# Performance work log

Measured on AMD Instinct MI355X. Metric: run time of the kernel, lower is better.

## Reference

```python
import jax, jax.numpy as jnp
import numpy as np

VOCAB = 50257
EMB = 100
BOT = 5  # bottleneck dim of the tiny autoencoder MLP


def setup_inputs() -> dict:
    key = jax.random.key(0)
    ks = jax.random.split(key, 7)
    B, S = 128, 2048
    x = jax.random.randint(ks[0], (B, S), 0, VOCAB, dtype=jnp.int64)
    word_embed = jax.random.normal(ks[1], (VOCAB, EMB), dtype=jnp.float32)
    # idf values are positive; use uniform(0,1] scaled up a bit to mimic log-idf
    idf = jax.random.uniform(ks[2], (VOCAB,), dtype=jnp.float32, minval=0.01, maxval=10.0)
    fc1_w = jax.random.normal(ks[3], (BOT, EMB), dtype=jnp.float32) * (1.0 / np.sqrt(EMB))
    fc1_b = jax.random.normal(ks[4], (BOT,), dtype=jnp.float32) * 0.01
    fc2_w = jax.random.normal(ks[5], (EMB, BOT), dtype=jnp.float32) * (1.0 / np.sqrt(BOT))
    fc2_b = jax.random.normal(ks[6], (EMB,), dtype=jnp.float32) * 0.01
    return {"x": x, "word_embed": word_embed, "idf": idf,
            "fc1_w": fc1_w, "fc1_b": fc1_b, "fc2_w": fc2_w, "fc2_b": fc2_b}


def reference(x, word_embed, idf, fc1_w, fc1_b, fc2_w, fc2_b):
    B, S = x.shape
    V = idf.shape[0]
    # tf(): per-row token histogram. Equivalent math to the torch dense
    # one-hot scatter + sum over seq, done as a scatter-add (no (B,S,V) tensor).
    rows = jnp.broadcast_to(jnp.arange(B)[:, None], (B, S))
    tf = jnp.zeros((B, V), dtype=jnp.float32).at[rows, x].add(1.0)
    # tf-idf weights, row-normalized
    tfidf = tf * idf[None, :]
    tfidf = tfidf / jnp.sum(tfidf, axis=1, keepdims=True)
    # per-token weight: gather each row's tfidf at its token ids  -> [B, S]
    w = jnp.take_along_axis(tfidf, x, axis=1)
    # embedding lookup and tfidf-weighted sum over seq  -> [B, EMB]
    emb = word_embed[x]  # [B, S, EMB]
    doc = jnp.einsum('bse,bs->be', emb, w)
    # tiny 100 -> 5 -> 100 MLP (no nonlinearity in the original)
    h = doc @ fc1_w.T + fc1_b
    out = h @ fc2_w.T + fc2_b
    return out
```

## Files before the change

### kernel.cpp

```cpp
#include <hip/hip_runtime.h>

#define SEQ   2048
#define HALF  1024
#define EMB   100
#define BOT   5
#define HSIZE 4096
#define FT    1024
#define NW    16
#define GW    12
#define GTOK  76
#define HTOK  28

__global__ __launch_bounds__(FT) void kA_fused(
    const int* __restrict__ x, const float* __restrict__ idf,
    const float* __restrict__ we, float* __restrict__ partial,
    float* __restrict__ zhalf)
{
    __shared__ int   hkey[HSIZE];
    __shared__ int   hcnt[HSIZE];
    __shared__ int   skey[SEQ];
    __shared__ float sdup[HALF];
    __shared__ float part[NW][EMB];
    __shared__ float zred[NW];

    const int bx   = blockIdx.x;
    const int b    = bx >> 1;
    const int half = bx & 1;
    const int tid  = threadIdx.x;
    const int lane = tid & 63, wid = tid >> 6;
    const int vl   = (lane < EMB / 2) ? lane : 0;

    for (int i = tid; i < HSIZE; i += FT) { hkey[i] = -1; hcnt[i] = 0; }
    for (int i = tid; i < SEQ; i += FT) skey[i] = x[(size_t)b * SEQ + i];
    __syncthreads();

    if (wid >= GW) {
        const int ht = tid - GW * 64;
        for (int i = ht; i < SEQ; i += (NW - GW) * 64) {
            int key = skey[i];
            unsigned slot = ((unsigned)key * 2654435761u) >> 20;
            for (;;) {
                int prev = atomicCAS(&hkey[slot], -1, key);
                if (prev == -1 || prev == key) { atomicAdd(&hcnt[slot], 1); break; }
                slot = (slot + 1) & (HSIZE - 1);
            }
        }
    }

    const int hb    = half * HALF;
    const int start = (wid < GW) ? wid * GTOK : GW * GTOK + (wid - GW) * HTOK;
    const int end   = start + ((wid < GW) ? GTOK : HTOK);

    float accx, accy;
    float z = 0.0f;
    {
        float2 a0={0,0},a1={0,0},a2={0,0},a3={0,0},a4={0,0},a5={0,0},a6={0,0},a7={0,0};
        int i = start;
        for (; i + 8 <= end; i += 8) {
            int   k0=skey[hb+i+0], k1=skey[hb+i+1], k2=skey[hb+i+2], k3=skey[hb+i+3];
            int   k4=skey[hb+i+4], k5=skey[hb+i+5], k6=skey[hb+i+6], k7=skey[hb+i+7];
            float w0=idf[k0], w1=idf[k1], w2=idf[k2], w3=idf[k3];
            float w4=idf[k4], w5=idf[k5], w6=idf[k6], w7=idf[k7];
            float2 v0=((const float2*)(we+(size_t)k0*EMB))[vl];
            float2 v1=((const float2*)(we+(size_t)k1*EMB))[vl];
            float2 v2=((const float2*)(we+(size_t)k2*EMB))[vl];
            float2 v3=((const float2*)(we+(size_t)k3*EMB))[vl];
            float2 v4=((const float2*)(we+(size_t)k4*EMB))[vl];
            float2 v5=((const float2*)(we+(size_t)k5*EMB))[vl];
            float2 v6=((const float2*)(we+(size_t)k6*EMB))[vl];
            float2 v7=((const float2*)(we+(size_t)k7*EMB))[vl];
            a0.x+=w0*v0.x; a0.y+=w0*v0.y;  a1.x+=w1*v1.x; a1.y+=w1*v1.y;
            a2.x+=w2*v2.x; a2.y+=w2*v2.y;  a3.x+=w3*v3.x; a3.y+=w3*v3.y;
            a4.x+=w4*v4.x; a4.y+=w4*v4.y;  a5.x+=w5*v5.x; a5.y+=w5*v5.y;
            a6.x+=w6*v6.x; a6.y+=w6*v6.y;  a7.x+=w7*v7.x; a7.y+=w7*v7.y;
            z += ((w0+w1)+(w2+w3)) + ((w4+w5)+(w6+w7));
        }
        for (; i < end; ++i) {
            int k = skey[hb+i];
            float w = idf[k];
            float2 v = ((const float2*)(we+(size_t)k*EMB))[vl];
            a0.x += w*v.x; a0.y += w*v.y; z += w;
        }
        accx = ((a0.x+a1.x)+(a2.x+a3.x)) + ((a4.x+a5.x)+(a6.x+a7.x));
        accy = ((a0.y+a1.y)+(a2.y+a3.y)) + ((a4.y+a5.y)+(a6.y+a7.y));
    }
    if (lane == 0) zred[wid] = z;
    __syncthreads();

    {
        int k = skey[hb + tid];
        unsigned slot = ((unsigned)k * 2654435761u) >> 20;
        while (hkey[slot] != k) slot = (slot + 1) & (HSIZE - 1);
        int c = hcnt[slot];
        sdup[tid] = (c > 1) ? (float)(c - 1) * idf[k] : 0.0f;
    }
    __syncthreads();

    {
        float wl = sdup[wid * 64 + lane];
        int   kl = skey[hb + wid * 64 + lane];
        unsigned long long m = __ballot(wl != 0.0f);
        while (m) {
            int src = __ffsll((long long)m) - 1;  m &= m - 1;
            float w = __shfl(wl, src);
            int   k = __shfl(kl, src);
            float2 v = ((const float2*)(we + (size_t)k * EMB))[vl];
            accx += w * v.x; accy += w * v.y;
        }
    }
    if (lane < EMB / 2) { part[wid][2*lane] = accx; part[wid][2*lane+1] = accy; }
    __syncthreads();

    if (tid < EMB) {
        float a = 0.0f;
        #pragma unroll
        for (int w = 0; w < NW; ++w) a += part[w][tid];
        partial[(size_t)bx * EMB + tid] = a;
    }
    if (tid == 0) {
        float t = 0.0f;
        #pragma unroll
        for (int w = 0; w < NW; ++w) t += zred[w];
        zhalf[bx] = t;
    }
}

__global__ __launch_bounds__(128) void kB_mlp(
    const float* __restrict__ partial, const float* __restrict__ zhalf,
    const float* __restrict__ fc1w, const float* __restrict__ fc1b,
    const float* __restrict__ fc2w, const float* __restrict__ fc2b,
    float* __restrict__ out)
{
    __shared__ float doc[EMB];
    __shared__ float hsh[BOT];

    const int b = blockIdx.x, tid = threadIdx.x;
    const float iz = 1.0f / (zhalf[2*b] + zhalf[2*b+1]);

    if (tid < EMB) {
        const float* p = partial + (size_t)b * 2 * EMB + tid;
        doc[tid] = (p[0] + p[EMB]) * iz;
    }
    __syncthreads();

    if (tid < BOT) {
        float h = fc1b[tid];
        const float* wr = fc1w + tid * EMB;
        for (int e = 0; e < EMB; ++e) h += doc[e] * wr[e];
        hsh[tid] = h;
    }
    __syncthreads();

    if (tid < EMB) {
        float o = fc2b[tid];
        const float* wr = fc2w + tid * BOT;
        #pragma unroll
        for (int j = 0; j < BOT; ++j) o += hsh[j] * wr[j];
        out[(size_t)b * EMB + tid] = o;
    }
}

extern "C" void kernel_launch(void* const* d_in, const int* in_sizes, int n_in,
                              void* d_out, int out_size, void* d_ws, size_t ws_size,
                              hipStream_t stream) {
    const int*   x    = (const int*)d_in[0];
    const float* we   = (const float*)d_in[1];
    const float* idf  = (const float*)d_in[2];
    const float* fc1w = (const float*)d_in[3];
    const float* fc1b = (const float*)d_in[4];
    const float* fc2w = (const float*)d_in[5];
    const float* fc2b = (const float*)d_in[6];
    float*       out  = (float*)d_out;

    const int B = in_sizes[0] / SEQ;

    char*  ws      = (char*)d_ws;
    float* zhalf   = (float*)ws;
    float* partial = (float*)(ws + 4096);

    kA_fused<<<B * 2, FT,  0, stream>>>(x, idf, we, partial, zhalf);
    kB_mlp  <<<B,     128, 0, stream>>>(partial, zhalf, fc1w, fc1b, fc2w, fc2b, out);
}
```

Baseline: 98.29 us.

## Restructure histogram and gather: all warps hash, float4 gathers, cached idf in LDS

Every thread now inserts two tokens into the shared hash table and keeps their slots, so the separate lookup probe pass is gone. The idf values are loaded once into shared memory and the normaliser is reduced with wave shuffles. The embedding gather switches from float2 to float4 loads, with two tokens per wave (25 lanes each), spread evenly over all 16 warps. Each block now computes the full-row normaliser redundantly, so the second kernel reads it directly. Duplicate correction leaves lanes 25-63 idle, and shared memory use grows.

```diff
diff --git a/kernel.cpp b/kernel.cpp
--- a/kernel.cpp
+++ b/kernel.cpp
@@ -7,126 +7,136 @@
 #define HSIZE 4096
 #define FT    1024
 #define NW    16
-#define GW    12
-#define GTOK  76
-#define HTOK  28
 
 __global__ __launch_bounds__(FT) void kA_fused(
     const int* __restrict__ x, const float* __restrict__ idf,
     const float* __restrict__ we, float* __restrict__ partial,
-    float* __restrict__ zhalf)
+    float* __restrict__ zfull)
 {
     __shared__ int   hkey[HSIZE];
     __shared__ int   hcnt[HSIZE];
     __shared__ int   skey[SEQ];
+    __shared__ float sidf[SEQ];
     __shared__ float sdup[HALF];
-    __shared__ float part[NW][EMB];
+    __shared__ float part[NW][2][EMB];
     __shared__ float zred[NW];
 
-    const int bx   = blockIdx.x;
-    const int b    = bx >> 1;
-    const int half = bx & 1;
-    const int tid  = threadIdx.x;
-    const int lane = tid & 63, wid = tid >> 6;
-    const int vl   = (lane < EMB / 2) ? lane : 0;
+    const int bx = blockIdx.x, b = bx >> 1, half = bx & 1;
+    const int tid = threadIdx.x, lane = tid & 63, wid = tid >> 6;
 
     for (int i = tid; i < HSIZE; i += FT) { hkey[i] = -1; hcnt[i] = 0; }
-    for (int i = tid; i < SEQ; i += FT) skey[i] = x[(size_t)b * SEQ + i];
+    skey[tid]        = x[(size_t)b * SEQ + tid];
+    skey[tid + HALF] = x[(size_t)b * SEQ + tid + HALF];
     __syncthreads();
 
-    if (wid >= GW) {
-        const int ht = tid - GW * 64;
-        for (int i = ht; i < SEQ; i += (NW - GW) * 64) {
-            int key = skey[i];
-            unsigned slot = ((unsigned)key * 2654435761u) >> 20;
-            for (;;) {
-                int prev = atomicCAS(&hkey[slot], -1, key);
-                if (prev == -1 || prev == key) { atomicAdd(&hcnt[slot], 1); break; }
-                slot = (slot + 1) & (HSIZE - 1);
+    const int   k0 = skey[tid], k1 = skey[tid + HALF];
+    const float w0 = idf[k0],   w1 = idf[k1];
+
+    unsigned slot0 = ((unsigned)k0 * 2654435761u) >> 20;
+    for (;;) {
+        int prev = atomicCAS(&hkey[slot0], -1, k0);
+        if (prev == -1 || prev == k0) { atomicAdd(&hcnt[slot0], 1); break; }
+        slot0 = (slot0 + 1) & (HSIZE - 1);
+    }
+    unsigned slot1 = ((unsigned)k1 * 2654435761u) >> 20;
+    for (;;) {
+        int prev = atomicCAS(&hkey[slot1], -1, k1);
+        if (prev == -1 || prev == k1) { atomicAdd(&hcnt[slot1], 1); break; }
+        slot1 = (slot1 + 1) & (HSIZE - 1);
+    }
+
+    sidf[tid] = w0;  sidf[tid + HALF] = w1;
+
+    float z = w0 + w1;
+    for (int off = 32; off > 0; off >>= 1) z += __shfl_down(z, off);
+    if (lane == 0) zred[wid] = z;
+    __syncthreads();
+
+    {
+        const int   ms = half ? (int)slot1 : (int)slot0;
+        const float mw = half ? w1 : w0;
+        const int   c  = hcnt[ms];
+        sdup[tid] = (c > 1) ? (float)(c - 1) * mw : 0.0f;
+    }
+    if (tid == 0) {
+        float t = 0.0f;
+        #pragma unroll
+        for (int i = 0; i < NW; ++i) t += zred[i];
+        zfull[b] = t;
+    }
+    __syncthreads();
+
+    const int  hb  = half * HALF;
+    const bool act = (lane < 50);
+    const int  sub = (lane < 25) ? 0 : 1;
+    const int  q   = (lane < 25) ? lane : lane - 25;
+
+    float4 a0={0,0,0,0}, a1={0,0,0,0}, a2={0,0,0,0}, a3={0,0,0,0};
+    float4 a4={0,0,0,0}, a5={0,0,0,0}, a6={0,0,0,0}, a7={0,0,0,0};
+
+    if (act) {
+        const int t0 = hb + wid * 64 + sub;
+        #pragma unroll
+        for (int it = 0; it < 4; ++it) {
+            const int base = t0 + it * 16;
+            int   kk0 = skey[base+ 0], kk1 = skey[base+ 2], kk2 = skey[base+ 4], kk3 = skey[base+ 6];
+            int   kk4 = skey[base+ 8], kk5 = skey[base+10], kk6 = skey[base+12], kk7 = skey[base+14];
+            float ww0 = sidf[base+ 0], ww1 = sidf[base+ 2], ww2 = sidf[base+ 4], ww3 = sidf[base+ 6];
+            float ww4 = sidf[base+ 8], ww5 = sidf[base+10], ww6 = sidf[base+12], ww7 = sidf[base+14];
+            float4 v0 = ((const float4*)(we + (size_t)kk0 * EMB))[q];
+            float4 v1 = ((const float4*)(we + (size_t)kk1 * EMB))[q];
+            float4 v2 = ((const float4*)(we + (size_t)kk2 * EMB))[q];
+            float4 v3 = ((const float4*)(we + (size_t)kk3 * EMB))[q];
+            float4 v4 = ((const float4*)(we + (size_t)kk4 * EMB))[q];
+            float4 v5 = ((const float4*)(we + (size_t)kk5 * EMB))[q];
+            float4 v6 = ((const float4*)(we + (size_t)kk6 * EMB))[q];
+            float4 v7 = ((const float4*)(we + (size_t)kk7 * EMB))[q];
+            a0.x+=ww0*v0.x; a0.y+=ww0*v0.y; a0.z+=ww0*v0.z; a0.w+=ww0*v0.w;
+            a1.x+=ww1*v1.x; a1.y+=ww1*v1.y; a1.z+=ww1*v1.z; a1.w+=ww1*v1.w;
+            a2.x+=ww2*v2.x; a2.y+=ww2*v2.y; a2.z+=ww2*v2.z; a2.w+=ww2*v2.w;
+            a3.x+=ww3*v3.x; a3.y+=ww3*v3.y; a3.z+=ww3*v3.z; a3.w+=ww3*v3.w;
+            a4.x+=ww4*v4.x; a4.y+=ww4*v4.y; a4.z+=ww4*v4.z; a4.w+=ww4*v4.w;
+            a5.x+=ww5*v5.x; a5.y+=ww5*v5.y; a5.z+=ww5*v5.z; a5.w+=ww5*v5.w;
+            a6.x+=ww6*v6.x; a6.y+=ww6*v6.y; a6.z+=ww6*v6.z; a6.w+=ww6*v6.w;
+            a7.x+=ww7*v7.x; a7.y+=ww7*v7.y; a7.z+=ww7*v7.z; a7.w+=ww7*v7.w;
+        }
+    }
+
+    {
+        float sd = sdup[wid * 64 + lane];
+        int   kl = skey[hb + wid * 64 + lane];
+        unsigned long long m = __ballot(sd != 0.0f);
+        while (m) {
+            int src = __ffsll((long long)m) - 1;  m &= m - 1;
+            float wv = __shfl(sd, src);
+            int   kv = __shfl(kl, src);
+            if (lane < 25) {
+                float4 v = ((const float4*)(we + (size_t)kv * EMB))[q];
+                a0.x += wv*v.x; a0.y += wv*v.y; a0.z += wv*v.z; a0.w += wv*v.w;
             }
         }
     }
 
-    const int hb    = half * HALF;
-    const int start = (wid < GW) ? wid * GTOK : GW * GTOK + (wid - GW) * HTOK;
-    const int end   = start + ((wid < GW) ? GTOK : HTOK);
-
-    float accx, accy;
-    float z = 0.0f;
-    {
-        float2 a0={0,0},a1={0,0},a2={0,0},a3={0,0},a4={0,0},a5={0,0},a6={0,0},a7={0,0};
-        int i = start;
-        for (; i + 8 <= end; i += 8) {
-            int   k0=skey[hb+i+0], k1=skey[hb+i+1], k2=skey[hb+i+2], k3=skey[hb+i+3];
-            int   k4=skey[hb+i+4], k5=skey[hb+i+5], k6=skey[hb+i+6], k7=skey[hb+i+7];
-            float w0=idf[k0], w1=idf[k1], w2=idf[k2], w3=idf[k3];
-            float w4=idf[k4], w5=idf[k5], w6=idf[k6], w7=idf[k7];
-            float2 v0=((const float2*)(we+(size_t)k0*EMB))[vl];
-            float2 v1=((const float2*)(we+(size_t)k1*EMB))[vl];
-            float2 v2=((const float2*)(we+(size_t)k2*EMB))[vl];
-            float2 v3=((const float2*)(we+(size_t)k3*EMB))[vl];
-            float2 v4=((const float2*)(we+(size_t)k4*EMB))[vl];
-            float2 v5=((const float2*)(we+(size_t)k5*EMB))[vl];
-            float2 v6=((const float2*)(we+(size_t)k6*EMB))[vl];
-            float2 v7=((const float2*)(we+(size_t)k7*EMB))[vl];
-            a0.x+=w0*v0.x; a0.y+=w0*v0.y;  a1.x+=w1*v1.x; a1.y+=w1*v1.y;
-            a2.x+=w2*v2.x; a2.y+=w2*v2.y;  a3.x+=w3*v3.x; a3.y+=w3*v3.y;
-            a4.x+=w4*v4.x; a4.y+=w4*v4.y;  a5.x+=w5*v5.x; a5.y+=w5*v5.y;
-            a6.x+=w6*v6.x; a6.y+=w6*v6.y;  a7.x+=w7*v7.x; a7.y+=w7*v7.y;
-            z += ((w0+w1)+(w2+w3)) + ((w4+w5)+(w6+w7));
-        }
-        for (; i < end; ++i) {
-            int k = skey[hb+i];
-            float w = idf[k];
-            float2 v = ((const float2*)(we+(size_t)k*EMB))[vl];
-            a0.x += w*v.x; a0.y += w*v.y; z += w;
-        }
-        accx = ((a0.x+a1.x)+(a2.x+a3.x)) + ((a4.x+a5.x)+(a6.x+a7.x));
-        accy = ((a0.y+a1.y)+(a2.y+a3.y)) + ((a4.y+a5.y)+(a6.y+a7.y));
+    if (act) {
+        float4 s;
+        s.x = ((a0.x+a1.x)+(a2.x+a3.x)) + ((a4.x+a5.x)+(a6.x+a7.x));
+        s.y = ((a0.y+a1.y)+(a2.y+a3.y)) + ((a4.y+a5.y)+(a6.y+a7.y));
+        s.z = ((a0.z+a1.z)+(a2.z+a3.z)) + ((a4.z+a5.z)+(a6.z+a7.z));
+        s.w = ((a0.w+a1.w)+(a2.w+a3.w)) + ((a4.w+a5.w)+(a6.w+a7.w));
+        ((float4*)part[wid][sub])[q] = s;
     }
-    if (lane == 0) zred[wid] = z;
-    __syncthreads();
-
-    {
-        int k = skey[hb + tid];
-        unsigned slot = ((unsigned)k * 2654435761u) >> 20;
-        while (hkey[slot] != k) slot = (slot + 1) & (HSIZE - 1);
-        int c = hcnt[slot];
-        sdup[tid] = (c > 1) ? (float)(c - 1) * idf[k] : 0.0f;
-    }
-    __syncthreads();
-
-    {
-        float wl = sdup[wid * 64 + lane];
-        int   kl = skey[hb + wid * 64 + lane];
-        unsigned long long m = __ballot(wl != 0.0f);
-        while (m) {
-            int src = __ffsll((long long)m) - 1;  m &= m - 1;
-            float w = __shfl(wl, src);
-            int   k = __shfl(kl, src);
-            float2 v = ((const float2*)(we + (size_t)k * EMB))[vl];
-            accx += w * v.x; accy += w * v.y;
-        }
-    }
-    if (lane < EMB / 2) { part[wid][2*lane] = accx; part[wid][2*lane+1] = accy; }
     __syncthreads();
 
     if (tid < EMB) {
         float a = 0.0f;
         #pragma unroll
-        for (int w = 0; w < NW; ++w) a += part[w][tid];
+        for (int w = 0; w < NW; ++w) a += part[w][0][tid] + part[w][1][tid];
         partial[(size_t)bx * EMB + tid] = a;
-    }
-    if (tid == 0) {
-        float t = 0.0f;
-        #pragma unroll
-        for (int w = 0; w < NW; ++w) t += zred[w];
-        zhalf[bx] = t;
     }
 }
 
 __global__ __launch_bounds__(128) void kB_mlp(
-    const float* __restrict__ partial, const float* __restrict__ zhalf,
+    const float* __restrict__ partial, const float* __restrict__ zfull,
     const float* __restrict__ fc1w, const float* __restrict__ fc1b,
     const float* __restrict__ fc2w, const float* __restrict__ fc2b,
     float* __restrict__ out)
@@ -135,7 +145,7 @@
     __shared__ float hsh[BOT];
 
     const int b = blockIdx.x, tid = threadIdx.x;
-    const float iz = 1.0f / (zhalf[2*b] + zhalf[2*b+1]);
+    const float iz = 1.0f / zfull[b];
 
     if (tid < EMB) {
         const float* p = partial + (size_t)b * 2 * EMB + tid;
@@ -175,9 +185,9 @@
     const int B = in_sizes[0] / SEQ;
 
     char*  ws      = (char*)d_ws;
-    float* zhalf   = (float*)ws;
+    float* zfull   = (float*)ws;
     float* partial = (float*)(ws + 4096);
 
-    kA_fused<<<B * 2, FT,  0, stream>>>(x, idf, we, partial, zhalf);
-    kB_mlp  <<<B,     128, 0, stream>>>(partial, zhalf, fc1w, fc1b, fc2w, fc2b, out);
+    kA_fused<<<B * 2, FT,  0, stream>>>(x, idf, we, partial, zfull);
+    kB_mlp  <<<B,     128, 0, stream>>>(partial, zfull, fc1w, fc1b, fc2w, fc2b, out);
 }
```

New measurement: 98.95 us. No clear change (+0.7%).
